# Optimization experiments

Hardware: AMD Instinct MI355X
Metric: run time of the kernel (lower is better)

The kernel has to match this reference:

```python
import jax, jax.numpy as jnp
import numpy as np

N_NODES = 50000

def _gcn_layer(h, src, dst, norm, W, activate):
    # symmetric-normalized aggregation: D^-1/2 A D^-1/2 h, then linear
    h = h * norm[:, None]                      # [N, d] pre-scale
    msg = h[src]                               # gather over edges [E, d]
    agg = jax.ops.segment_sum(msg, dst, num_segments=N_NODES)  # scatter-add
    h = agg * norm[:, None]                    # post-scale
    h = h @ W
    return jax.nn.relu(h) if activate else h


def setup_inputs() -> dict:
    key = jax.random.key(0)
    k1, k2, k3, k4, k5, k6 = jax.random.split(key, 6)
    d_in, d_hid, d_out, n_edges = 128, 128, 40, 640000
    features = jax.random.normal(k1, (N_NODES, d_in), dtype=jnp.float32)
    edge_index = jax.random.randint(k2, (2, n_edges), 0, N_NODES, dtype=jnp.int64)
    s = 1.0 / np.sqrt(d_hid)
    W0 = jax.random.normal(k3, (d_in, d_hid), dtype=jnp.float32) * s
    W1 = jax.random.normal(k4, (d_hid, d_hid), dtype=jnp.float32) * s
    W2 = jax.random.normal(k5, (d_hid, d_hid), dtype=jnp.float32) * s
    W3 = jax.random.normal(k6, (d_hid, d_out), dtype=jnp.float32) * s
    return {"features": features, "edge_index": edge_index,
            "W0": W0, "W1": W1, "W2": W2, "W3": W3}


def reference(features, edge_index, W0, W1, W2, W3):
    src, dst = edge_index[0], edge_index[1]
    # in-degree based symmetric norm (graph_norm=True), clamp isolated nodes
    deg = jax.ops.segment_sum(jnp.ones_like(dst, dtype=features.dtype), dst,
                              num_segments=N_NODES)
    norm = jax.lax.rsqrt(jnp.maximum(deg, 1.0))
    h = features
    h = _gcn_layer(h, src, dst, norm, W0, True)
    h = _gcn_layer(h, src, dst, norm, W1, True)
    h = _gcn_layer(h, src, dst, norm, W2, True)
    h = _gcn_layer(h, src, dst, norm, W3, False)  # last layer: no activation
    return h
```

## Files before the change

### kernel.cpp

```cpp
#include <hip/hip_runtime.h>
#include <hip/hip_fp16.h>


#define DIM 128
#define CHUNK 1024
#define HS_LD 136

typedef __attribute__((ext_vector_type(8))) _Float16 f16x8;
typedef __attribute__((ext_vector_type(4))) float f32x4;

__global__ void deg_kernel(const int* __restrict__ dst, int* __restrict__ deg, int E) {
    int i = blockIdx.x * blockDim.x + threadIdx.x;
    if (i < E) atomicAdd(&deg[dst[i]], 1);
}

__global__ __launch_bounds__(256) void scanA_kernel(
        const int* __restrict__ deg, float* __restrict__ nrm,
        int* __restrict__ bsum, int n) {
    int b = blockIdx.x, t = threadIdx.x;
    int base = b * CHUNK + t * 4;
    int s = 0;
    if (base + 3 < n) {
        int4 d = *(const int4*)&deg[base];
        s = d.x + d.y + d.z + d.w;
        float4 r;
        r.x = rsqrtf(fmaxf((float)d.x, 1.0f));
        r.y = rsqrtf(fmaxf((float)d.y, 1.0f));
        r.z = rsqrtf(fmaxf((float)d.z, 1.0f));
        r.w = rsqrtf(fmaxf((float)d.w, 1.0f));
        *(float4*)&nrm[base] = r;
    } else {
        for (int j = 0; j < 4; ++j) {
            int idx = base + j;
            if (idx < n) {
                int d = deg[idx];
                s += d;
                nrm[idx] = rsqrtf(fmaxf((float)d, 1.0f));
            }
        }
    }
    for (int o = 32; o; o >>= 1) s += __shfl_down(s, o, 64);
    __shared__ int ws[4];
    if ((t & 63) == 0) ws[t >> 6] = s;
    __syncthreads();
    if (t == 0) bsum[b] = ws[0] + ws[1] + ws[2] + ws[3];
}

__global__ __launch_bounds__(256) void scanBC_kernel(
        const int* __restrict__ deg, const int* __restrict__ bsum,
        int* __restrict__ off, int* __restrict__ cur, int n, int G) {
    __shared__ int pbs;
    __shared__ int wsum[4];
    int b = blockIdx.x, t = threadIdx.x;
    if (t < 64) {
        int orig = (t < G) ? bsum[t] : 0;
        int v = orig;
        for (int o = 1; o < 64; o <<= 1) {
            int u = __shfl_up(v, o, 64);
            if (t >= o) v += u;
        }
        if (b == 0 && t == G - 1) off[n] = v;
        if (t == b) pbs = v - orig;
    }
    int base = b * CHUNK + t * 4;
    if (base + 3 < n) *(int4*)&cur[base] = make_int4(0, 0, 0, 0);
    else for (int j = 0; j < 4; ++j) if (base + j < n) cur[base + j] = 0;

    int d0 = 0, d1 = 0, d2 = 0, d3 = 0;
    if (base + 3 < n) {
        int4 d = *(const int4*)&deg[base];
        d0 = d.x; d1 = d.y; d2 = d.z; d3 = d.w;
    } else {
        if (base     < n) d0 = deg[base];
        if (base + 1 < n) d1 = deg[base + 1];
        if (base + 2 < n) d2 = deg[base + 2];
    }
    int tot = d0 + d1 + d2 + d3;
    int v = tot;
    for (int o = 1; o < 64; o <<= 1) {
        int u = __shfl_up(v, o, 64);
        if ((t & 63) >= o) v += u;
    }
    if ((t & 63) == 63) wsum[t >> 6] = v;
    __syncthreads();
    int wbase = 0;
    for (int w = 0; w < (t >> 6); ++w) wbase += wsum[w];
    int p = pbs + wbase + (v - tot);
    if (base + 3 < n) {
        int4 o4 = make_int4(p, p + d0, p + d0 + d1, p + d0 + d1 + d2);
        *(int4*)&off[base] = o4;
    } else {
        if (base     < n) off[base]     = p;
        if (base + 1 < n) off[base + 1] = p + d0;
        if (base + 2 < n) off[base + 2] = p + d0 + d1;
    }
}

__global__ void fill_kernel(const int* __restrict__ src, const int* __restrict__ dst,
                            const int* __restrict__ off, int* __restrict__ cur,
                            int* __restrict__ csr, int E) {
    int i = blockIdx.x * blockDim.x + threadIdx.x;
    if (i < E) {
        int d = dst[i];
        int p = atomicAdd(&cur[d], 1);
        csr[off[d] + p] = src[i];
    }
}

__global__ void prep_kernel(const float* __restrict__ f, const float* __restrict__ nrm,
                            const float* __restrict__ W0, const float* __restrict__ W1,
                            const float* __restrict__ W2, const float* __restrict__ W3,
                            __half* __restrict__ featH, __half* __restrict__ Wt,
                            int n4) {
    int i = blockIdx.x * blockDim.x + threadIdx.x;
    if (i < n4) {
        int r = i >> 5, c4 = i & 31;
        float s = nrm[r];
        float4 v = ((const float4*)f)[i];
        __half2 lo = __float22half2_rn(make_float2(v.x * s, v.y * s));
        __half2 hi = __float22half2_rn(make_float2(v.z * s, v.w * s));
        uint2 u;
        u.x = *(unsigned int*)&lo;
        u.y = *(unsigned int*)&hi;
        *(uint2*)&featH[(size_t)r * DIM + c4 * 4] = u;
    } else {
        int w = i - n4;
        if (w < 3 * 128 * 128) {
            int l = w >> 14, c = (w >> 7) & 127, k = w & 127;
            const float* W = (l == 0) ? W0 : ((l == 1) ? W1 : W2);
            Wt[w] = __float2half(W[k * 128 + c]);
        } else if (w < 3 * 128 * 128 + 48 * 128) {
            int j = w - 3 * 128 * 128;
            int c = j >> 7, k = j & 127;
            Wt[w] = __float2half((c < 40) ? W3[k * 40 + c] : 0.f);
        }
    }
}

__global__ __launch_bounds__(256) void aggh_kernel(
        const __half* __restrict__ hin, const float* __restrict__ nrm,
        const int* __restrict__ off, const int* __restrict__ csr,
        __half* __restrict__ out, int N) {
    int t = threadIdx.x;
    int lane = t & 63;
    int node = blockIdx.x * 4 + (t >> 6);
    if (node >= N) return;
    int pos = lane & 15, sg = lane >> 4;
    int c = pos * 8;
    int b = off[node], e = off[node + 1];
    float a[8] = {0,0,0,0,0,0,0,0};
    float bb[8] = {0,0,0,0,0,0,0,0};
    int j = b + sg;
    for (; j + 4 < e; j += 8) {
        int s0 = csr[j], s1 = csr[j + 4];
        uint4 u0 = *(const uint4*)&hin[(size_t)s0 * DIM + c];
        uint4 u1 = *(const uint4*)&hin[(size_t)s1 * DIM + c];
        float2 f;
        f = __half22float2(*(__half2*)&u0.x); a[0]+=f.x; a[1]+=f.y;
        f = __half22float2(*(__half2*)&u0.y); a[2]+=f.x; a[3]+=f.y;
        f = __half22float2(*(__half2*)&u0.z); a[4]+=f.x; a[5]+=f.y;
        f = __half22float2(*(__half2*)&u0.w); a[6]+=f.x; a[7]+=f.y;
        f = __half22float2(*(__half2*)&u1.x); bb[0]+=f.x; bb[1]+=f.y;
        f = __half22float2(*(__half2*)&u1.y); bb[2]+=f.x; bb[3]+=f.y;
        f = __half22float2(*(__half2*)&u1.z); bb[4]+=f.x; bb[5]+=f.y;
        f = __half22float2(*(__half2*)&u1.w); bb[6]+=f.x; bb[7]+=f.y;
    }
    for (; j < e; j += 4) {
        uint4 u = *(const uint4*)&hin[(size_t)csr[j] * DIM + c];
        float2 f;
        f = __half22float2(*(__half2*)&u.x); a[0]+=f.x; a[1]+=f.y;
        f = __half22float2(*(__half2*)&u.y); a[2]+=f.x; a[3]+=f.y;
        f = __half22float2(*(__half2*)&u.z); a[4]+=f.x; a[5]+=f.y;
        f = __half22float2(*(__half2*)&u.w); a[6]+=f.x; a[7]+=f.y;
    }
#pragma unroll
    for (int k = 0; k < 8; ++k) a[k] += bb[k];
#pragma unroll
    for (int k = 0; k < 8; ++k) {
        a[k] += __shfl_xor(a[k], 16, 64);
        a[k] += __shfl_xor(a[k], 32, 64);
    }
    if (sg == 0) {
        float s = nrm[node];
        __half2 h0 = __float22half2_rn(make_float2(a[0]*s, a[1]*s));
        __half2 h1 = __float22half2_rn(make_float2(a[2]*s, a[3]*s));
        __half2 h2 = __float22half2_rn(make_float2(a[4]*s, a[5]*s));
        __half2 h3 = __float22half2_rn(make_float2(a[6]*s, a[7]*s));
        uint4 u;
        u.x = *(unsigned int*)&h0; u.y = *(unsigned int*)&h1;
        u.z = *(unsigned int*)&h2; u.w = *(unsigned int*)&h3;
        *(uint4*)&out[(size_t)node * DIM + c] = u;
    }
}

__global__ __launch_bounds__(256) void gemmM_kernel(
        const __half* __restrict__ Ah, const __half* __restrict__ Wt,
        const float* __restrict__ nrm, __half* __restrict__ outh, int n) {
    int t = threadIdx.x;
    int lane = t & 63, wv = t >> 6;
    int row0 = blockIdx.x * 64 + wv * 16;
    int arow = row0 + (lane & 15);
    int ar = (arow < n) ? arow : (n - 1);
    int kg = lane >> 4;

    const __half* Abase = Ah + (size_t)ar * DIM + kg * 8;
    f16x8 a[4];
#pragma unroll
    for (int k0 = 0; k0 < 4; ++k0)
        a[k0] = *(const f16x8*)(Abase + k0 * 32);

    f32x4 acc[8];
#pragma unroll
    for (int ct = 0; ct < 8; ++ct) {
        acc[ct] = (f32x4){0.f, 0.f, 0.f, 0.f};
        const __half* Bbase = Wt + (size_t)(ct * 16 + (lane & 15)) * DIM + kg * 8;
#pragma unroll
        for (int k0 = 0; k0 < 4; ++k0) {
            f16x8 b = *(const f16x8*)(Bbase + k0 * 32);
            acc[ct] = __builtin_amdgcn_mfma_f32_16x16x32_f16(a[k0], b, acc[ct], 0, 0, 0);
        }
    }

    int col = lane & 15;
    int rbase = row0 + (lane >> 4) * 4;
#pragma unroll
    for (int r = 0; r < 4; ++r) {
        int row = rbase + r;
        if (row >= n) continue;
        float s = nrm[row];
#pragma unroll
        for (int ct = 0; ct < 8; ++ct) {
            float v = fmaxf(acc[ct][r], 0.f) * s;
            outh[(size_t)row * DIM + ct * 16 + col] = __float2half(v);
        }
    }
}

__global__ __launch_bounds__(256) void gemmM2_kernel(
        const __half* __restrict__ Ah, const __half* __restrict__ Wt2,
        const __half* __restrict__ Wt3, const float* __restrict__ nrm,
        __half* __restrict__ g3h, int n) {
    __shared__ __half Hs[64 * HS_LD];
    int t = threadIdx.x;
    int lane = t & 63, wv = t >> 6;
    int row0 = blockIdx.x * 64 + wv * 16;
    int arow = row0 + (lane & 15);
    int ar = (arow < n) ? arow : (n - 1);
    int kg = lane >> 4;

    const __half* Abase = Ah + (size_t)ar * DIM + kg * 8;
    f16x8 a[4];
#pragma unroll
    for (int k0 = 0; k0 < 4; ++k0)
        a[k0] = *(const f16x8*)(Abase + k0 * 32);

    f32x4 acc[8];
#pragma unroll
    for (int ct = 0; ct < 8; ++ct) {
        acc[ct] = (f32x4){0.f, 0.f, 0.f, 0.f};
        const __half* Bbase = Wt2 + (size_t)(ct * 16 + (lane & 15)) * DIM + kg * 8;
#pragma unroll
        for (int k0 = 0; k0 < 4; ++k0) {
            f16x8 b = *(const f16x8*)(Bbase + k0 * 32);
            acc[ct] = __builtin_amdgcn_mfma_f32_16x16x32_f16(a[k0], b, acc[ct], 0, 0, 0);
        }
    }

    int col = lane & 15;
    int lr0 = wv * 16 + (lane >> 4) * 4;
#pragma unroll
    for (int r = 0; r < 4; ++r) {
        int lrow = lr0 + r;
        int grow = blockIdx.x * 64 + lrow;
        float s = (grow < n) ? nrm[grow] : 0.f;
#pragma unroll
        for (int ct = 0; ct < 8; ++ct) {
            float v = fmaxf(acc[ct][r], 0.f) * s;
            Hs[lrow * HS_LD + ct * 16 + col] = __float2half(v);
        }
    }
    __syncthreads();

    int lrowA = wv * 16 + (lane & 15);
    const __half* Hbase = &Hs[lrowA * HS_LD + kg * 8];
    f16x8 a2[4];
#pragma unroll
    for (int k0 = 0; k0 < 4; ++k0)
        a2[k0] = *(const f16x8*)(Hbase + k0 * 32);

    f32x4 acc2[3];
#pragma unroll
    for (int ct = 0; ct < 3; ++ct) {
        acc2[ct] = (f32x4){0.f, 0.f, 0.f, 0.f};
        const __half* Bbase = Wt3 + (size_t)(ct * 16 + (lane & 15)) * DIM + kg * 8;
#pragma unroll
        for (int k0 = 0; k0 < 4; ++k0) {
            f16x8 b = *(const f16x8*)(Bbase + k0 * 32);
            acc2[ct] = __builtin_amdgcn_mfma_f32_16x16x32_f16(a2[k0], b, acc2[ct], 0, 0, 0);
        }
    }

    int rbase = row0 + (lane >> 4) * 4;
#pragma unroll
    for (int r = 0; r < 4; ++r) {
        int row = rbase + r;
        if (row >= n) continue;
#pragma unroll
        for (int ct = 0; ct < 3; ++ct) {
            int cc = ct * 16 + col;
            if (cc < 40)
                g3h[(size_t)row * 40 + cc] = __float2half(acc2[ct][r]);
        }
    }
}

__global__ __launch_bounds__(256) void agg40_kernel(
        const __half* __restrict__ hin, const float* __restrict__ nrm,
        const int* __restrict__ off, const int* __restrict__ csr,
        float* __restrict__ out, int N) {
    int t = threadIdx.x;
    int lane = t & 63, wv = t >> 6;
    int g = lane >> 4, pos = lane & 15;
    int node = blockIdx.x * 16 + wv * 4 + g;
    if (node >= N || pos >= 10) return;
    int b = off[node], e = off[node + 1];
    float4 a0 = make_float4(0,0,0,0), a1 = a0, a2 = a0, a3 = a0;
    int j = b;
    for (; j + 3 < e; j += 4) {
        int s0 = csr[j], s1 = csr[j+1], s2 = csr[j+2], s3 = csr[j+3];
        uint2 u0 = *(const uint2*)&hin[(size_t)s0 * 40 + pos * 4];
        uint2 u1 = *(const uint2*)&hin[(size_t)s1 * 40 + pos * 4];
        uint2 u2 = *(const uint2*)&hin[(size_t)s2 * 40 + pos * 4];
        uint2 u3 = *(const uint2*)&hin[(size_t)s3 * 40 + pos * 4];
        float2 f;
        f = __half22float2(*(__half2*)&u0.x); a0.x+=f.x; a0.y+=f.y;
        f = __half22float2(*(__half2*)&u0.y); a0.z+=f.x; a0.w+=f.y;
        f = __half22float2(*(__half2*)&u1.x); a1.x+=f.x; a1.y+=f.y;
        f = __half22float2(*(__half2*)&u1.y); a1.z+=f.x; a1.w+=f.y;
        f = __half22float2(*(__half2*)&u2.x); a2.x+=f.x; a2.y+=f.y;
        f = __half22float2(*(__half2*)&u2.y); a2.z+=f.x; a2.w+=f.y;
        f = __half22float2(*(__half2*)&u3.x); a3.x+=f.x; a3.y+=f.y;
        f = __half22float2(*(__half2*)&u3.y); a3.z+=f.x; a3.w+=f.y;
    }
    for (; j < e; ++j) {
        uint2 u = *(const uint2*)&hin[(size_t)csr[j] * 40 + pos * 4];
        float2 f;
        f = __half22float2(*(__half2*)&u.x); a0.x+=f.x; a0.y+=f.y;
        f = __half22float2(*(__half2*)&u.y); a0.z+=f.x; a0.w+=f.y;
    }
    float s = nrm[node];
    float4 r;
    r.x = ((a0.x+a1.x) + (a2.x+a3.x)) * s;
    r.y = ((a0.y+a1.y) + (a2.y+a3.y)) * s;
    r.z = ((a0.z+a1.z) + (a2.z+a3.z)) * s;
    r.w = ((a0.w+a1.w) + (a2.w+a3.w)) * s;
    *(float4*)&out[(size_t)node * 40 + pos * 4] = r;
}

extern "C" void kernel_launch(void* const* d_in, const int* in_sizes, int n_in,
                              void* d_out, int out_size, void* d_ws, size_t ws_size,
                              hipStream_t stream) {
    const float* features = (const float*)d_in[0];
    const int*   edges    = (const int*)d_in[1];
    const float* W0       = (const float*)d_in[2];
    const float* W1       = (const float*)d_in[3];
    const float* W2       = (const float*)d_in[4];
    const float* W3       = (const float*)d_in[5];

    const int N = in_sizes[0] / DIM;
    const int E = in_sizes[1] / 2;
    const int* src = edges;
    const int* dst = edges + E;

    char* p = (char*)d_ws;
    __half* featH = (__half*)p; p += (size_t)N * DIM * 2;
    __half* agg16 = (__half*)p; p += (size_t)N * DIM * 2;
    __half* h16   = (__half*)p; p += (size_t)N * DIM * 2;
    __half* g3h   = (__half*)p; p += (size_t)N * 64 * 2;
    __half* Wt    = (__half*)p; p += (size_t)(3 * 128 * 128 + 48 * 128) * 2;
    float*  nrm   = (float*)p;  p += (size_t)N * 4;
    int*    deg   = (int*)p;    p += (size_t)N * 4;
    int*    cur   = (int*)p;    p += (size_t)N * 4;
    int*    off   = (int*)p;    p += (size_t)(N + 1) * 4;
    int*    bsum  = (int*)p;    p += 64 * 4;
    int*    csr   = (int*)p;    p += (size_t)E * 4;
    (void)ws_size; (void)n_in; (void)out_size;

    hipMemsetAsync(deg, 0, (size_t)N * sizeof(int), stream);

    int eb = (E + 255) / 256;
    int G  = (N + CHUNK - 1) / CHUNK;
    deg_kernel   <<<eb, 256, 0, stream>>>(dst, deg, E);
    scanA_kernel <<<G, 256, 0, stream>>>(deg, nrm, bsum, N);
    scanBC_kernel<<<G, 256, 0, stream>>>(deg, bsum, off, cur, N, G);
    fill_kernel  <<<eb, 256, 0, stream>>>(src, dst, off, cur, csr, E);

    int n4 = N * (DIM / 4);
    int prepTot = n4 + 3 * 128 * 128 + 48 * 128;
    prep_kernel<<<(prepTot + 255) / 256, 256, 0, stream>>>(
        features, nrm, W0, W1, W2, W3, featH, Wt, n4);

    int gb = (N + 63) / 64;
    int ab = (N + 3) / 4;
    aggh_kernel<<<ab, 256, 0, stream>>>(featH, nrm, off, csr, agg16, N);
    gemmM_kernel<<<gb, 256, 0, stream>>>(agg16, Wt, nrm, h16, N);

    aggh_kernel<<<ab, 256, 0, stream>>>(h16, nrm, off, csr, agg16, N);
    gemmM_kernel<<<gb, 256, 0, stream>>>(agg16, Wt + 128 * 128, nrm, h16, N);

    aggh_kernel<<<ab, 256, 0, stream>>>(h16, nrm, off, csr, agg16, N);
    gemmM2_kernel<<<gb, 256, 0, stream>>>(agg16, Wt + 2 * 128 * 128,
                                          Wt + 3 * 128 * 128, nrm, g3h, N);

    agg40_kernel<<<(N + 15) / 16, 256, 0, stream>>>(g3h, nrm, off, csr,
                                                    (float*)d_out, N);
}
```

Before: 252.3 us.

## Fuse scan offsets with feature/weight prep and pad layer-4 rows to 64

Merges the offset-scan kernel with the fp16 feature and weight conversion into one grid-stride kernel, removing one launch and letting the prep work run alongside the scan blocks. It also pads the layer-4 intermediate rows from 40 to 64 halves so gathers are aligned, and keeps all lanes alive in agg40 until the store. The padding adds gather traffic per edge and extra zero writes, and the fused kernel uses a fixed grid of 392 blocks.

```diff
diff --git a/kernel.cpp b/kernel.cpp
--- a/kernel.cpp
+++ b/kernel.cpp
@@ -46,74 +46,66 @@
     if (t == 0) bsum[b] = ws[0] + ws[1] + ws[2] + ws[3];
 }
 
-__global__ __launch_bounds__(256) void scanBC_kernel(
+__global__ __launch_bounds__(256) void scanBCprep_kernel(
         const int* __restrict__ deg, const int* __restrict__ bsum,
-        int* __restrict__ off, int* __restrict__ cur, int n, int G) {
+        int* __restrict__ off, int* __restrict__ cur,
+        const float* __restrict__ f, const float* __restrict__ nrm,
+        const float* __restrict__ W0, const float* __restrict__ W1,
+        const float* __restrict__ W2, const float* __restrict__ W3,
+        __half* __restrict__ featH, __half* __restrict__ Wt,
+        int n, int G) {
     __shared__ int pbs;
     __shared__ int wsum[4];
     int b = blockIdx.x, t = threadIdx.x;
-    if (t < 64) {
-        int orig = (t < G) ? bsum[t] : 0;
-        int v = orig;
+    if (b < G) {
+        if (t < 64) {
+            int orig = (t < G) ? bsum[t] : 0;
+            int v = orig;
+            for (int o = 1; o < 64; o <<= 1) {
+                int u = __shfl_up(v, o, 64);
+                if (t >= o) v += u;
+            }
+            if (b == 0 && t == G - 1) off[n] = v;
+            if (t == b) pbs = v - orig;
+        }
+        int base = b * CHUNK + t * 4;
+        if (base + 3 < n) *(int4*)&cur[base] = make_int4(0, 0, 0, 0);
+        else for (int j = 0; j < 4; ++j) if (base + j < n) cur[base + j] = 0;
+
+        int d0 = 0, d1 = 0, d2 = 0, d3 = 0;
+        if (base + 3 < n) {
+            int4 d = *(const int4*)&deg[base];
+            d0 = d.x; d1 = d.y; d2 = d.z; d3 = d.w;
+        } else {
+            if (base     < n) d0 = deg[base];
+            if (base + 1 < n) d1 = deg[base + 1];
+            if (base + 2 < n) d2 = deg[base + 2];
+        }
+        int tot = d0 + d1 + d2 + d3;
+        int v = tot;
         for (int o = 1; o < 64; o <<= 1) {
             int u = __shfl_up(v, o, 64);
-            if (t >= o) v += u;
-        }
-        if (b == 0 && t == G - 1) off[n] = v;
-        if (t == b) pbs = v - orig;
-    }
-    int base = b * CHUNK + t * 4;
-    if (base + 3 < n) *(int4*)&cur[base] = make_int4(0, 0, 0, 0);
-    else for (int j = 0; j < 4; ++j) if (base + j < n) cur[base + j] = 0;
-
-    int d0 = 0, d1 = 0, d2 = 0, d3 = 0;
-    if (base + 3 < n) {
-        int4 d = *(const int4*)&deg[base];
-        d0 = d.x; d1 = d.y; d2 = d.z; d3 = d.w;
-    } else {
-        if (base     < n) d0 = deg[base];
-        if (base + 1 < n) d1 = deg[base + 1];
-        if (base + 2 < n) d2 = deg[base + 2];
-    }
-    int tot = d0 + d1 + d2 + d3;
-    int v = tot;
-    for (int o = 1; o < 64; o <<= 1) {
-        int u = __shfl_up(v, o, 64);
-        if ((t & 63) >= o) v += u;
-    }
-    if ((t & 63) == 63) wsum[t >> 6] = v;
-    __syncthreads();
-    int wbase = 0;
-    for (int w = 0; w < (t >> 6); ++w) wbase += wsum[w];
-    int p = pbs + wbase + (v - tot);
-    if (base + 3 < n) {
-        int4 o4 = make_int4(p, p + d0, p + d0 + d1, p + d0 + d1 + d2);
-        *(int4*)&off[base] = o4;
-    } else {
-        if (base     < n) off[base]     = p;
-        if (base + 1 < n) off[base + 1] = p + d0;
-        if (base + 2 < n) off[base + 2] = p + d0 + d1;
-    }
-}
-
-__global__ void fill_kernel(const int* __restrict__ src, const int* __restrict__ dst,
-                            const int* __restrict__ off, int* __restrict__ cur,
-                            int* __restrict__ csr, int E) {
-    int i = blockIdx.x * blockDim.x + threadIdx.x;
-    if (i < E) {
-        int d = dst[i];
-        int p = atomicAdd(&cur[d], 1);
-        csr[off[d] + p] = src[i];
-    }
-}
-
-__global__ void prep_kernel(const float* __restrict__ f, const float* __restrict__ nrm,
-                            const float* __restrict__ W0, const float* __restrict__ W1,
-                            const float* __restrict__ W2, const float* __restrict__ W3,
-                            __half* __restrict__ featH, __half* __restrict__ Wt,
-                            int n4) {
-    int i = blockIdx.x * blockDim.x + threadIdx.x;
-    if (i < n4) {
+            if ((t & 63) >= o) v += u;
+        }
+        if ((t & 63) == 63) wsum[t >> 6] = v;
+        __syncthreads();
+        int wbase = 0;
+        for (int w = 0; w < (t >> 6); ++w) wbase += wsum[w];
+        int p = pbs + wbase + (v - tot);
+        if (base + 3 < n) {
+            int4 o4 = make_int4(p, p + d0, p + d0 + d1, p + d0 + d1 + d2);
+            *(int4*)&off[base] = o4;
+        } else {
+            if (base     < n) off[base]     = p;
+            if (base + 1 < n) off[base + 1] = p + d0;
+            if (base + 2 < n) off[base + 2] = p + d0 + d1;
+        }
+    }
+
+    int gtid = b * 256 + t;
+    int gsz = gridDim.x * 256;
+    int n4 = n * 32;
+    for (int i = gtid; i < n4; i += gsz) {
         int r = i >> 5, c4 = i & 31;
         float s = nrm[r];
         float4 v = ((const float4*)f)[i];
@@ -123,17 +115,29 @@
         u.x = *(unsigned int*)&lo;
         u.y = *(unsigned int*)&hi;
         *(uint2*)&featH[(size_t)r * DIM + c4 * 4] = u;
-    } else {
-        int w = i - n4;
+    }
+    const int WTOT = 3 * 128 * 128 + 48 * 128;
+    for (int w = gtid; w < WTOT; w += gsz) {
         if (w < 3 * 128 * 128) {
             int l = w >> 14, c = (w >> 7) & 127, k = w & 127;
             const float* W = (l == 0) ? W0 : ((l == 1) ? W1 : W2);
             Wt[w] = __float2half(W[k * 128 + c]);
-        } else if (w < 3 * 128 * 128 + 48 * 128) {
+        } else {
             int j = w - 3 * 128 * 128;
             int c = j >> 7, k = j & 127;
             Wt[w] = __float2half((c < 40) ? W3[k * 40 + c] : 0.f);
         }
+    }
+}
+
+__global__ void fill_kernel(const int* __restrict__ src, const int* __restrict__ dst,
+                            const int* __restrict__ off, int* __restrict__ cur,
+                            int* __restrict__ csr, int E) {
+    int i = blockIdx.x * blockDim.x + threadIdx.x;
+    if (i < E) {
+        int d = dst[i];
+        int p = atomicAdd(&cur[d], 1);
+        csr[off[d] + p] = src[i];
     }
 }
 
@@ -306,11 +310,9 @@
         int row = rbase + r;
         if (row >= n) continue;
 #pragma unroll
-        for (int ct = 0; ct < 3; ++ct) {
-            int cc = ct * 16 + col;
-            if (cc < 40)
-                g3h[(size_t)row * 40 + cc] = __float2half(acc2[ct][r]);
-        }
+        for (int ct = 0; ct < 3; ++ct)
+            g3h[(size_t)row * 64 + ct * 16 + col] = __float2half(acc2[ct][r]);
+        g3h[(size_t)row * 64 + 48 + col] = __float2half(0.f);
     }
 }
 
@@ -322,16 +324,16 @@
     int lane = t & 63, wv = t >> 6;
     int g = lane >> 4, pos = lane & 15;
     int node = blockIdx.x * 16 + wv * 4 + g;
-    if (node >= N || pos >= 10) return;
+    if (node >= N) return;
     int b = off[node], e = off[node + 1];
     float4 a0 = make_float4(0,0,0,0), a1 = a0, a2 = a0, a3 = a0;
     int j = b;
     for (; j + 3 < e; j += 4) {
         int s0 = csr[j], s1 = csr[j+1], s2 = csr[j+2], s3 = csr[j+3];
-        uint2 u0 = *(const uint2*)&hin[(size_t)s0 * 40 + pos * 4];
-        uint2 u1 = *(const uint2*)&hin[(size_t)s1 * 40 + pos * 4];
-        uint2 u2 = *(const uint2*)&hin[(size_t)s2 * 40 + pos * 4];
-        uint2 u3 = *(const uint2*)&hin[(size_t)s3 * 40 + pos * 4];
+        uint2 u0 = *(const uint2*)&hin[(size_t)s0 * 64 + pos * 4];
+        uint2 u1 = *(const uint2*)&hin[(size_t)s1 * 64 + pos * 4];
+        uint2 u2 = *(const uint2*)&hin[(size_t)s2 * 64 + pos * 4];
+        uint2 u3 = *(const uint2*)&hin[(size_t)s3 * 64 + pos * 4];
         float2 f;
         f = __half22float2(*(__half2*)&u0.x); a0.x+=f.x; a0.y+=f.y;
         f = __half22float2(*(__half2*)&u0.y); a0.z+=f.x; a0.w+=f.y;
@@ -343,11 +345,12 @@
         f = __half22float2(*(__half2*)&u3.y); a3.z+=f.x; a3.w+=f.y;
     }
     for (; j < e; ++j) {
-        uint2 u = *(const uint2*)&hin[(size_t)csr[j] * 40 + pos * 4];
+        uint2 u = *(const uint2*)&hin[(size_t)csr[j] * 64 + pos * 4];
         float2 f;
         f = __half22float2(*(__half2*)&u.x); a0.x+=f.x; a0.y+=f.y;
         f = __half22float2(*(__half2*)&u.y); a0.z+=f.x; a0.w+=f.y;
     }
+    if (pos >= 10) return;
     float s = nrm[node];
     float4 r;
     r.x = ((a0.x+a1.x) + (a2.x+a3.x)) * s;
@@ -390,15 +393,12 @@
 
     int eb = (E + 255) / 256;
     int G  = (N + CHUNK - 1) / CHUNK;
-    deg_kernel   <<<eb, 256, 0, stream>>>(dst, deg, E);
-    scanA_kernel <<<G, 256, 0, stream>>>(deg, nrm, bsum, N);
-    scanBC_kernel<<<G, 256, 0, stream>>>(deg, bsum, off, cur, N, G);
-    fill_kernel  <<<eb, 256, 0, stream>>>(src, dst, off, cur, csr, E);
-
-    int n4 = N * (DIM / 4);
-    int prepTot = n4 + 3 * 128 * 128 + 48 * 128;
-    prep_kernel<<<(prepTot + 255) / 256, 256, 0, stream>>>(
-        features, nrm, W0, W1, W2, W3, featH, Wt, n4);
+    deg_kernel  <<<eb, 256, 0, stream>>>(dst, deg, E);
+    scanA_kernel<<<G, 256, 0, stream>>>(deg, nrm, bsum, N);
+    scanBCprep_kernel<<<392, 256, 0, stream>>>(deg, bsum, off, cur,
+                                               features, nrm, W0, W1, W2, W3,
+                                               featH, Wt, N, G);
+    fill_kernel <<<eb, 256, 0, stream>>>(src, dst, off, cur, csr, E);
 
     int gb = (N + 63) / 64;
     int ab = (N + 3) / 4;
```

Measured after the change: 249.0 us. About the same (-1.3%).
